# Optimization experiments

Measured on AMD Instinct MI355X. Metric: run time of the kernel, lower is better.

Reference implementation:

```python
import jax, jax.numpy as jnp
import numpy as np

INPUT_DIM = 128
OUTPUT_DIM = 32
H1, H2 = 32, 16

def _lstm(x, Wih, Whh, bih, bhh):
    # x: [B,T,D]; Wih: [4H,D]; Whh: [4H,H]; PyTorch gate order i,f,g,o
    B = x.shape[0]
    H = Whh.shape[1]
    xg = jnp.einsum('btd,gd->btg', x, Wih) + bih + bhh  # precompute input gates [B,T,4H]
    def step(carry, g):
        h, c = carry
        gates = g + h @ Whh.T
        i, f, gg, o = jnp.split(gates, 4, axis=-1)
        c = jax.nn.sigmoid(f) * c + jax.nn.sigmoid(i) * jnp.tanh(gg)
        h = jax.nn.sigmoid(o) * jnp.tanh(c)
        return (h, c), h
    h0 = jnp.zeros((B, H), x.dtype)
    (_, _), hs = jax.lax.scan(step, (h0, h0), jnp.swapaxes(xg, 0, 1))
    return jnp.swapaxes(hs, 0, 1)  # [B,T,H]

def setup_inputs() -> dict:
    key = jax.random.key(0)
    ks = jax.random.split(key, 16)
    def rn(k, shape, scale=0.05):
        return jax.random.normal(k, shape, dtype=jnp.float32) * scale
    d = {}
    d['x'] = jax.random.normal(ks[0], (512, INPUT_DIM, 1024), dtype=jnp.float32)
    d['conv_w'] = rn(ks[1], (INPUT_DIM, INPUT_DIM, 5))
    d['conv_b'] = rn(ks[2], (INPUT_DIM,))
    d['Wih1'] = rn(ks[3], (4 * H1, INPUT_DIM)); d['Whh1'] = rn(ks[4], (4 * H1, H1))
    d['bih1'] = rn(ks[5], (4 * H1,));          d['bhh1'] = rn(ks[6], (4 * H1,))
    d['Wih2'] = rn(ks[7], (4 * H2, H1));       d['Whh2'] = rn(ks[8], (4 * H2, H2))
    d['bih2'] = rn(ks[9], (4 * H2,));          d['bhh2'] = rn(ks[10], (4 * H2,))
    d['Wih3'] = rn(ks[11], (4 * OUTPUT_DIM, H2)); d['Whh3'] = rn(ks[12], (4 * OUTPUT_DIM, OUTPUT_DIM))
    d['bih3'] = rn(ks[13], (4 * OUTPUT_DIM,));    d['bhh3'] = rn(ks[14], (4 * OUTPUT_DIM,))
    return d

def reference(x, conv_w, conv_b, Wih1, Whh1, bih1, bhh1, Wih2, Whh2, bih2, bhh2, Wih3, Whh3, bih3, bhh3):
    B = x.shape[0]
    t = x.reshape(B, INPUT_DIM, -1)
    c = jax.lax.conv_general_dilated(t, conv_w, window_strides=(1,), padding='VALID',
                                     dimension_numbers=('NCH', 'OIH', 'NCH'))
    c = c + conv_b[None, :, None]  # [B, C, L']
    # faithful to torch .view: reshape (not transpose) to [B, L', C]
    seq = c.reshape(B, -1, c.shape[1])
    h1 = _lstm(seq, Wih1, Whh1, bih1, bhh1)
    h2 = _lstm(h1, Wih2, Whh2, bih2, bhh2)
    h3 = _lstm(h2, Wih3, Whh3, bih3, bhh3)
    return h3[:, -1, :]
```

## Files before the change

### kernel.cpp

```cpp
#include <hip/hip_runtime.h>

static constexpr int BATCH = 512;
static constexpr int TT    = 1020;
static constexpr int MM    = BATCH * TT;

typedef __bf16 bf8 __attribute__((ext_vector_type(8)));
typedef float  f4v __attribute__((ext_vector_type(4)));

__device__ __forceinline__ float fsig(float x) {
  float e = __builtin_amdgcn_exp2f(x * -1.442695041f);
  return __builtin_amdgcn_rcpf(1.0f + e);
}
__device__ __forceinline__ float ftanh(float x) {
  float e = __builtin_amdgcn_exp2f(x * 2.885390082f);
  return 1.0f - 2.0f * __builtin_amdgcn_rcpf(e + 1.0f);
}

__device__ __forceinline__ f4v mfma16(bf8 a, bf8 b, f4v c) {
  return __builtin_amdgcn_mfma_f32_16x16x32_bf16(a, b, c, 0, 0, 0);
}

__global__ __launch_bounds__(64) void pack_w_kernel(
    const float* __restrict__ w, ushort* __restrict__ wp) {
  const int lane = threadIdx.x;
  const int ch = blockIdx.x & 3;
  const int ct = (blockIdx.x >> 2) & 7;
  const int k  = blockIdx.x >> 5;
  const int co  = ct * 16 + (lane & 15);
  const int ci0 = ch * 32 + (lane >> 4) * 8;
  ushort hi[8], lo[8];
#pragma unroll
  for (int j = 0; j < 8; ++j) {
    const float v = w[(size_t)(co * 128 + ci0 + j) * 5 + k];
    const unsigned u = __float_as_uint(v);
    const float hf = __uint_as_float(u & 0xffff0000u);
    hi[j] = (ushort)(u >> 16);
    lo[j] = (ushort)(__float_as_uint(v - hf) >> 16);
  }
  ushort* d0 = wp + ((size_t)blockIdx.x * 2 + 0) * 512 + (size_t)lane * 8;
  ushort* d1 = d0 + 512;
#pragma unroll
  for (int j = 0; j < 8; ++j) { d0[j] = hi[j]; d1[j] = lo[j]; }
}

__global__ __launch_bounds__(256) void conv_mfma_kernel(
    const float* __restrict__ x, const ushort* __restrict__ wp,
    const float* __restrict__ bias, float* __restrict__ c) {
  __shared__ ushort xT[2][260][40];
  const int b    = blockIdx.z;
  const int cb   = blockIdx.x;
  const int l0   = blockIdx.y * 256;
  const int tid  = threadIdx.x;
  const int lane = tid & 63;
  const int wv   = tid >> 6;
  const int lrow = lane & 15;
  const int lgrp = lane >> 4;

  f4v acc[4][4];
#pragma unroll
  for (int m = 0; m < 4; ++m)
#pragma unroll
    for (int t = 0; t < 4; ++t) acc[m][t] = (f4v){0.f, 0.f, 0.f, 0.f};

  const int sp  = tid & 15;
  const int slq = tid >> 4;

  for (int ch = 0; ch < 4; ++ch) {
    const int ci0 = ch * 32;
    __syncthreads();
    {
      const float* xr0 = x + ((size_t)b * 128 + ci0 + 2 * sp) * 1024 + l0;
      const float* xr1 = xr0 + 1024;
      for (int j = 0; j < 5; ++j) {
        const int l = slq * 4 + 64 * j;
        if (l >= 260) break;
        const bool ok = (l0 + l) < 1024;
        float4 a0 = make_float4(0.f, 0.f, 0.f, 0.f);
        float4 a1 = make_float4(0.f, 0.f, 0.f, 0.f);
        if (ok) { a0 = *(const float4*)(xr0 + l); a1 = *(const float4*)(xr1 + l); }
        const float v0[4] = {a0.x, a0.y, a0.z, a0.w};
        const float v1[4] = {a1.x, a1.y, a1.z, a1.w};
#pragma unroll
        for (int e = 0; e < 4; ++e) {
          const unsigned u0 = __float_as_uint(v0[e]);
          const unsigned u1 = __float_as_uint(v1[e]);
          const unsigned h0 = u0 & 0xffff0000u;
          const unsigned h1 = u1 & 0xffff0000u;
          const float l0f = v0[e] - __uint_as_float(h0);
          const float l1f = v1[e] - __uint_as_float(h1);
          const unsigned hp = (u0 >> 16) | h1;
          const unsigned lp = (__float_as_uint(l0f) >> 16) |
                              (__float_as_uint(l1f) & 0xffff0000u);
          *(unsigned*)&xT[0][l + e][2 * sp] = hp;
          *(unsigned*)&xT[1][l + e][2 * sp] = lp;
        }
      }
    }
    __syncthreads();
#pragma unroll
    for (int k = 0; k < 5; ++k) {
      bf8 xa[4][2];
#pragma unroll
      for (int m = 0; m < 4; ++m) {
        const int row = wv * 64 + m * 16 + lrow + k;
        xa[m][0] = *(const bf8*)&xT[0][row][lgrp * 8];
        xa[m][1] = *(const bf8*)&xT[1][row][lgrp * 8];
      }
#pragma unroll
      for (int ct = 0; ct < 4; ++ct) {
        const ushort* wf =
            wp + (size_t)(((k * 8 + cb * 4 + ct) * 4 + ch) * 2) * 512 + lane * 8;
        const bf8 wh = *(const bf8*)wf;
        const bf8 wl = *(const bf8*)(wf + 512);
#pragma unroll
        for (int m = 0; m < 4; ++m) {
          acc[m][ct] = mfma16(xa[m][0], wh, acc[m][ct]);
          acc[m][ct] = mfma16(xa[m][1], wh, acc[m][ct]);
          acc[m][ct] = mfma16(xa[m][0], wl, acc[m][ct]);
        }
      }
    }
  }
#pragma unroll
  for (int ct = 0; ct < 4; ++ct) {
    const int co = cb * 64 + ct * 16 + lrow;
    const float bv = bias[co];
    float* crow = c + (size_t)b * 130560 + (size_t)co * TT;
#pragma unroll
    for (int m = 0; m < 4; ++m) {
      const int l = l0 + wv * 64 + m * 16 + lgrp * 4;
      if (l < TT) {
        float4 st;
        st.x = acc[m][ct][0] + bv; st.y = acc[m][ct][1] + bv;
        st.z = acc[m][ct][2] + bv; st.w = acc[m][ct][3] + bv;
        *(float4*)(crow + l) = st;
      }
    }
  }
}

template <int K>
__global__ __launch_bounds__(256) void gemm_xg(
    const float* __restrict__ A, const float* __restrict__ W,
    const float* __restrict__ bih, const float* __restrict__ bhh,
    float* __restrict__ xgT, const int Ntot) {
  constexpr int KC = (K > 64) ? 64 : K;
  constexpr int LITEMS = (16 * KC) / 256 > 0 ? (16 * KC) / 256 : 1;
  __shared__ float At[KC][68];
  __shared__ float Wt[KC][68];
  const int m0 = blockIdx.x * 64;
  const int n0 = blockIdx.y * 64;
  const int tid = threadIdx.x;
  const int tn = tid & 15;
  const int tm = tid >> 4;

  float acc[4][4];
#pragma unroll
  for (int i = 0; i < 4; ++i)
#pragma unroll
    for (int j = 0; j < 4; ++j) acc[i][j] = 0.f;

  for (int kc = 0; kc < K; kc += KC) {
    __syncthreads();
#pragma unroll
    for (int it = 0; it < LITEMS; ++it) {
      const int i  = tid + it * 256;
      const int r  = i / (KC / 4);
      const int c4 = i % (KC / 4);
      const float4 v = *(const float4*)(A + (size_t)(m0 + r) * K + kc + c4 * 4);
      At[c4 * 4 + 0][r] = v.x; At[c4 * 4 + 1][r] = v.y;
      At[c4 * 4 + 2][r] = v.z; At[c4 * 4 + 3][r] = v.w;
    }
#pragma unroll
    for (int it = 0; it < LITEMS; ++it) {
      const int i  = tid + it * 256;
      const int r  = i / (KC / 4);
      const int c4 = i % (KC / 4);
      const float4 v = *(const float4*)(W + (size_t)(n0 + r) * K + kc + c4 * 4);
      Wt[c4 * 4 + 0][r] = v.x; Wt[c4 * 4 + 1][r] = v.y;
      Wt[c4 * 4 + 2][r] = v.z; Wt[c4 * 4 + 3][r] = v.w;
    }
    __syncthreads();
#pragma unroll 8
    for (int k = 0; k < KC; ++k) {
      const float4 av = *(const float4*)&At[k][tm * 4];
      const float4 wv = *(const float4*)&Wt[k][tn * 4];
      const float a[4] = {av.x, av.y, av.z, av.w};
      const float wr[4] = {wv.x, wv.y, wv.z, wv.w};
#pragma unroll
      for (int i = 0; i < 4; ++i)
#pragma unroll
        for (int j = 0; j < 4; ++j)
          acc[i][j] = fmaf(a[i], wr[j], acc[i][j]);
    }
  }
  float bv[4];
#pragma unroll
  for (int j = 0; j < 4; ++j)
    bv[j] = bih[n0 + tn * 4 + j] + bhh[n0 + tn * 4 + j];
#pragma unroll
  for (int i = 0; i < 4; ++i) {
    const int m  = m0 + tm * 4 + i;
    const int bb = (int)(((unsigned long long)m * 4311810306ULL) >> 42);
    const int t  = m - bb * TT;
    float* dst = xgT + ((size_t)bb * Ntot + n0 + tn * 4) * TT + t;
#pragma unroll
    for (int j = 0; j < 4; ++j) dst[(size_t)j * TT] = acc[i][j] + bv[j];
  }
}

template <int H, bool FINAL>
__global__ __launch_bounds__(64) void lstm_kernel(
    const float* __restrict__ xgT, const float* __restrict__ Whh,
    float* __restrict__ hout) {
  constexpr int G   = 4 * H;
  constexpr int GPL = G / 64;
  constexpr int KG  = H / 4;
  const int b    = blockIdx.x;
  const int lane = threadIdx.x;
  const int g0 = lane;
  const int g1 = lane + 64;

  float w0[H];
  float w1[GPL == 2 ? H : 1];
#pragma unroll
  for (int k = 0; k < H; ++k) {
    w0[k] = Whh[g0 * H + k];
    if constexpr (GPL == 2) w1[k] = Whh[g1 * H + k];
  }

  const float* p0 = xgT + ((size_t)b * G + g0) * TT;
  const float* p1 = xgT + ((size_t)b * G + (GPL == 2 ? g1 : g0)) * TT;

  float h = 0.f, c = 0.f;
  float4 cur0[4], cur1[4], nxt0[4], nxt1[4];
#pragma unroll
  for (int r = 0; r < 4; ++r) {
    cur0[r] = *(const float4*)(p0 + 4 * r);
    nxt0[r] = *(const float4*)(p0 + 16 + 4 * r);
    if constexpr (GPL == 2) {
      cur1[r] = *(const float4*)(p1 + 4 * r);
      nxt1[r] = *(const float4*)(p1 + 16 + 4 * r);
    }
  }

  for (int t16 = 0; t16 < TT; t16 += 16) {
#pragma unroll
    for (int r = 0; r < 4; ++r) {
      const int t4 = t16 + 4 * r;
      if (t4 >= TT) break;
#pragma unroll
      for (int s = 0; s < 4; ++s) {
        float q0[4], q1[4];
        q0[0] = ((const float*)&cur0[r])[s]; q0[1] = 0.f; q0[2] = 0.f; q0[3] = 0.f;
        if constexpr (GPL == 2) {
          q1[0] = ((const float*)&cur1[r])[s]; q1[1] = 0.f; q1[2] = 0.f; q1[3] = 0.f;
        }
#pragma unroll
        for (int g = 0; g < 4; ++g)
#pragma unroll
          for (int k8 = 0; k8 < KG; ++k8) {
            const int k = g * KG + k8;
            const float hk =
                __uint_as_float(__builtin_amdgcn_readlane(__float_as_uint(h), k));
            q0[g] = fmaf(w0[k], hk, q0[g]);
            if constexpr (GPL == 2) q1[g] = fmaf(w1[k], hk, q1[g]);
          }
        const float acc0 = (q0[0] + q0[1]) + (q0[2] + q0[3]);
        float acc1 = 0.f;
        if constexpr (GPL == 2) acc1 = (q1[0] + q1[1]) + (q1[2] + q1[3]);

        float iraw, fraw, graw, oraw;
        if constexpr (H == 32) {
          const float r0 = __shfl_xor(acc0, 32, 64);
          const float r1 = __shfl_xor(acc1, 32, 64);
          const bool hi = lane >= 32;
          iraw = hi ? r0 : acc0;
          fraw = hi ? acc0 : r0;
          graw = hi ? r1 : acc1;
          oraw = hi ? acc1 : r1;
        } else {
          const float x1 = __shfl_xor(acc0, 16, 64);
          const float x2 = __shfl_xor(acc0, 32, 64);
          const float x3 = __shfl_xor(acc0, 48, 64);
          const int q = lane >> 4;
          const float t0 = (q & 1) ? x1 : acc0;
          const float t1 = (q & 1) ? acc0 : x1;
          const float u0 = (q & 1) ? x3 : x2;
          const float u1 = (q & 1) ? x2 : x3;
          const bool hi2 = q >= 2;
          iraw = hi2 ? u0 : t0;
          fraw = hi2 ? u1 : t1;
          graw = hi2 ? t0 : u0;
          oraw = hi2 ? t1 : u1;
        }
        const float ig = fsig(iraw);
        const float fg = fsig(fraw);
        const float gg = ftanh(graw);
        const float og = fsig(oraw);
        c = fmaf(fg, c, ig * gg);
        h = og * ftanh(c);
        if constexpr (!FINAL) {
          if (lane < H) hout[((size_t)b * TT + (t4 + s)) * H + lane] = h;
        } else {
          if (t4 + s == TT - 1 && lane < H) hout[b * H + lane] = h;
        }
      }
    }
#pragma unroll
    for (int r = 0; r < 4; ++r) {
      cur0[r] = nxt0[r];
      if constexpr (GPL == 2) cur1[r] = nxt1[r];
      const int tp = t16 + 32 + 4 * r;
      if (tp < TT) {
        nxt0[r] = *(const float4*)(p0 + tp);
        if constexpr (GPL == 2) nxt1[r] = *(const float4*)(p1 + tp);
      }
    }
  }
}

extern "C" void kernel_launch(void* const* d_in, const int* in_sizes, int n_in,
                              void* d_out, int out_size, void* d_ws, size_t ws_size,
                              hipStream_t stream) {
  const float* x      = (const float*)d_in[0];
  const float* conv_w = (const float*)d_in[1];
  const float* conv_b = (const float*)d_in[2];
  const float* Wih1   = (const float*)d_in[3];
  const float* Whh1   = (const float*)d_in[4];
  const float* bih1   = (const float*)d_in[5];
  const float* bhh1   = (const float*)d_in[6];
  const float* Wih2   = (const float*)d_in[7];
  const float* Whh2   = (const float*)d_in[8];
  const float* bih2   = (const float*)d_in[9];
  const float* bhh2   = (const float*)d_in[10];
  const float* Wih3   = (const float*)d_in[11];
  const float* Whh3   = (const float*)d_in[12];
  const float* bih3   = (const float*)d_in[13];
  const float* bhh3   = (const float*)d_in[14];
  float* out = (float*)d_out;
  float* ws  = (float*)d_ws;

  float* c    = ws;
  float* xgT1 = ws + 66846720;
  float* h1   = ws + 133693440;
  float* xgT2 = c;
  float* h2   = h1;
  float* xgT3 = xgT1;
  ushort* wpack = (ushort*)h1;

  pack_w_kernel<<<160, 64, 0, stream>>>(conv_w, wpack);
  conv_mfma_kernel<<<dim3(2, 4, BATCH), 256, 0, stream>>>(x, wpack, conv_b, c);
  gemm_xg<128><<<dim3(MM / 64, 2), 256, 0, stream>>>(c, Wih1, bih1, bhh1, xgT1, 128);
  lstm_kernel<32, false><<<BATCH, 64, 0, stream>>>(xgT1, Whh1, h1);
  gemm_xg<32><<<dim3(MM / 64, 1), 256, 0, stream>>>(h1, Wih2, bih2, bhh2, xgT2, 64);
  lstm_kernel<16, false><<<BATCH, 64, 0, stream>>>(xgT2, Whh2, h2);
  gemm_xg<16><<<dim3(MM / 64, 2), 256, 0, stream>>>(h2, Wih3, bih3, bhh3, xgT3, 128);
  lstm_kernel<32, true><<<BATCH, 64, 0, stream>>>(xgT3, Whh3, out);
}
```

Baseline: 2.271 ms.

## Interleave multiple batch sequences per wavefront in LSTM recurrence kernels

Each LSTM block now processes NC batch elements (4 for H=32, 8 for H=16) with interleaved independent recurrences inside one wavefront, and the grid shrinks by the same factor. The goal is to hide the serial latency of readlane/FMA/transcendental chains by giving the scheduler independent work from other sequences. The input-gate prefetch is restructured into a 3-slot float4 ring buffer, and launch bounds now request one wave per SIMD. The trade-off is far fewer blocks than compute units, plus higher register pressure.

```diff
diff --git a/kernel.cpp b/kernel.cpp
--- a/kernel.cpp
+++ b/kernel.cpp
@@ -209,112 +209,128 @@
   }
 }
 
-template <int H, bool FINAL>
-__global__ __launch_bounds__(64) void lstm_kernel(
+template <int H, int NC, bool FINAL>
+__global__ __launch_bounds__(64, 1) void lstm_kernel(
     const float* __restrict__ xgT, const float* __restrict__ Whh,
     float* __restrict__ hout) {
   constexpr int G   = 4 * H;
   constexpr int GPL = G / 64;
   constexpr int KG  = H / 4;
-  const int b    = blockIdx.x;
+  const int b0   = blockIdx.x * NC;
   const int lane = threadIdx.x;
-  const int g0 = lane;
-  const int g1 = lane + 64;
 
   float w0[H];
   float w1[GPL == 2 ? H : 1];
 #pragma unroll
   for (int k = 0; k < H; ++k) {
-    w0[k] = Whh[g0 * H + k];
-    if constexpr (GPL == 2) w1[k] = Whh[g1 * H + k];
-  }
-
-  const float* p0 = xgT + ((size_t)b * G + g0) * TT;
-  const float* p1 = xgT + ((size_t)b * G + (GPL == 2 ? g1 : g0)) * TT;
-
-  float h = 0.f, c = 0.f;
-  float4 cur0[4], cur1[4], nxt0[4], nxt1[4];
-#pragma unroll
-  for (int r = 0; r < 4; ++r) {
-    cur0[r] = *(const float4*)(p0 + 4 * r);
-    nxt0[r] = *(const float4*)(p0 + 16 + 4 * r);
+    w0[k] = Whh[lane * H + k];
+    if constexpr (GPL == 2) w1[k] = Whh[(lane + 64) * H + k];
+  }
+
+  const float* p0[NC];
+  const float* p1[GPL == 2 ? NC : 1];
+  float hs[NC], cs[NC];
+  float4 buf0[NC][3];
+  float4 buf1[GPL == 2 ? NC : 1][3];
+#pragma unroll
+  for (int cc = 0; cc < NC; ++cc) {
+    p0[cc] = xgT + ((size_t)(b0 + cc) * G + lane) * TT;
+    hs[cc] = 0.f; cs[cc] = 0.f;
+#pragma unroll
+    for (int sl = 0; sl < 3; ++sl)
+      buf0[cc][sl] = *(const float4*)(p0[cc] + 4 * sl);
     if constexpr (GPL == 2) {
-      cur1[r] = *(const float4*)(p1 + 4 * r);
-      nxt1[r] = *(const float4*)(p1 + 16 + 4 * r);
-    }
-  }
-
-  for (int t16 = 0; t16 < TT; t16 += 16) {
-#pragma unroll
-    for (int r = 0; r < 4; ++r) {
-      const int t4 = t16 + 4 * r;
-      if (t4 >= TT) break;
-#pragma unroll
+      p1[cc] = xgT + ((size_t)(b0 + cc) * G + lane + 64) * TT;
+#pragma unroll
+      for (int sl = 0; sl < 3; ++sl)
+        buf1[cc][sl] = *(const float4*)(p1[cc] + 4 * sl);
+    }
+  }
+
+  for (int t12 = 0; t12 < TT; t12 += 12) {
+#pragma unroll
+    for (int sl = 0; sl < 3; ++sl) {
+#pragma unroll 1
       for (int s = 0; s < 4; ++s) {
-        float q0[4], q1[4];
-        q0[0] = ((const float*)&cur0[r])[s]; q0[1] = 0.f; q0[2] = 0.f; q0[3] = 0.f;
-        if constexpr (GPL == 2) {
-          q1[0] = ((const float*)&cur1[r])[s]; q1[1] = 0.f; q1[2] = 0.f; q1[3] = 0.f;
+        const int t = t12 + sl * 4 + s;
+#pragma unroll
+        for (int cc = 0; cc < NC; ++cc) {
+          const float4 v0 = buf0[cc][sl];
+          const float xg0 =
+              (s == 0) ? v0.x : (s == 1) ? v0.y : (s == 2) ? v0.z : v0.w;
+          float xg1 = 0.f;
+          if constexpr (GPL == 2) {
+            const float4 v1 = buf1[cc][sl];
+            xg1 = (s == 0) ? v1.x : (s == 1) ? v1.y : (s == 2) ? v1.z : v1.w;
+          }
+          float q0[4], q1[4];
+          q0[0] = xg0; q0[1] = 0.f; q0[2] = 0.f; q0[3] = 0.f;
+          if constexpr (GPL == 2) {
+            q1[0] = xg1; q1[1] = 0.f; q1[2] = 0.f; q1[3] = 0.f;
+          }
+#pragma unroll
+          for (int g = 0; g < 4; ++g)
+#pragma unroll
+            for (int k8 = 0; k8 < KG; ++k8) {
+              const int k = g * KG + k8;
+              const float hk = __uint_as_float(
+                  __builtin_amdgcn_readlane(__float_as_uint(hs[cc]), k));
+              q0[g] = fmaf(w0[k], hk, q0[g]);
+              if constexpr (GPL == 2) q1[g] = fmaf(w1[k], hk, q1[g]);
+            }
+          const float acc0 = (q0[0] + q0[1]) + (q0[2] + q0[3]);
+          float acc1 = 0.f;
+          if constexpr (GPL == 2) acc1 = (q1[0] + q1[1]) + (q1[2] + q1[3]);
+
+          float iraw, fraw, graw, oraw;
+          if constexpr (H == 32) {
+            const float r0 = __shfl_xor(acc0, 32, 64);
+            const float r1 = __shfl_xor(acc1, 32, 64);
+            const bool hi = lane >= 32;
+            iraw = hi ? r0 : acc0;
+            fraw = hi ? acc0 : r0;
+            graw = hi ? r1 : acc1;
+            oraw = hi ? acc1 : r1;
+          } else {
+            const float x1 = __shfl_xor(acc0, 16, 64);
+            const float x2 = __shfl_xor(acc0, 32, 64);
+            const float x3 = __shfl_xor(acc0, 48, 64);
+            const int q = lane >> 4;
+            const float t0 = (q & 1) ? x1 : acc0;
+            const float t1 = (q & 1) ? acc0 : x1;
+            const float u0 = (q & 1) ? x3 : x2;
+            const float u1 = (q & 1) ? x2 : x3;
+            const bool hi2 = q >= 2;
+            iraw = hi2 ? u0 : t0;
+            fraw = hi2 ? u1 : t1;
+            graw = hi2 ? t0 : u0;
+            oraw = hi2 ? t1 : u1;
+          }
+          const float ig = fsig(iraw);
+          const float fg = fsig(fraw);
+          const float gg = ftanh(graw);
+          const float og = fsig(oraw);
+          cs[cc] = fmaf(fg, cs[cc], ig * gg);
+          hs[cc] = og * ftanh(cs[cc]);
+          if constexpr (!FINAL) {
+            if (lane < H)
+              hout[((size_t)(b0 + cc) * TT + t) * H + lane] = hs[cc];
+          } else {
+            if (t == TT - 1 && lane < H)
+              hout[(b0 + cc) * H + lane] = hs[cc];
+          }
         }
-#pragma unroll
-        for (int g = 0; g < 4; ++g)
-#pragma unroll
-          for (int k8 = 0; k8 < KG; ++k8) {
-            const int k = g * KG + k8;
-            const float hk =
-                __uint_as_float(__builtin_amdgcn_readlane(__float_as_uint(h), k));
-            q0[g] = fmaf(w0[k], hk, q0[g]);
-            if constexpr (GPL == 2) q1[g] = fmaf(w1[k], hk, q1[g]);
-          }
-        const float acc0 = (q0[0] + q0[1]) + (q0[2] + q0[3]);
-        float acc1 = 0.f;
-        if constexpr (GPL == 2) acc1 = (q1[0] + q1[1]) + (q1[2] + q1[3]);
-
-        float iraw, fraw, graw, oraw;
-        if constexpr (H == 32) {
-          const float r0 = __shfl_xor(acc0, 32, 64);
-          const float r1 = __shfl_xor(acc1, 32, 64);
-          const bool hi = lane >= 32;
-          iraw = hi ? r0 : acc0;
-          fraw = hi ? acc0 : r0;
-          graw = hi ? r1 : acc1;
-          oraw = hi ? acc1 : r1;
-        } else {
-          const float x1 = __shfl_xor(acc0, 16, 64);
-          const float x2 = __shfl_xor(acc0, 32, 64);
-          const float x3 = __shfl_xor(acc0, 48, 64);
-          const int q = lane >> 4;
-          const float t0 = (q & 1) ? x1 : acc0;
-          const float t1 = (q & 1) ? acc0 : x1;
-          const float u0 = (q & 1) ? x3 : x2;
-          const float u1 = (q & 1) ? x2 : x3;
-          const bool hi2 = q >= 2;
-          iraw = hi2 ? u0 : t0;
-          fraw = hi2 ? u1 : t1;
-          graw = hi2 ? t0 : u0;
-          oraw = hi2 ? t1 : u1;
+      }
+      {
+        const int tp = t12 + 12 + 4 * sl;
+        if (tp < TT) {
+#pragma unroll
+          for (int cc = 0; cc < NC; ++cc) {
+            buf0[cc][sl] = *(const float4*)(p0[cc] + tp);
+            if constexpr (GPL == 2)
+              buf1[cc][sl] = *(const float4*)(p1[cc] + tp);
+          }
         }
-        const float ig = fsig(iraw);
-        const float fg = fsig(fraw);
-        const float gg = ftanh(graw);
-        const float og = fsig(oraw);
-        c = fmaf(fg, c, ig * gg);
-        h = og * ftanh(c);
-        if constexpr (!FINAL) {
-          if (lane < H) hout[((size_t)b * TT + (t4 + s)) * H + lane] = h;
-        } else {
-          if (t4 + s == TT - 1 && lane < H) hout[b * H + lane] = h;
-        }
-      }
-    }
-#pragma unroll
-    for (int r = 0; r < 4; ++r) {
-      cur0[r] = nxt0[r];
-      if constexpr (GPL == 2) cur1[r] = nxt1[r];
-      const int tp = t16 + 32 + 4 * r;
-      if (tp < TT) {
-        nxt0[r] = *(const float4*)(p0 + tp);
-        if constexpr (GPL == 2) nxt1[r] = *(const float4*)(p1 + tp);
       }
     }
   }
@@ -352,9 +368,9 @@
   pack_w_kernel<<<160, 64, 0, stream>>>(conv_w, wpack);
   conv_mfma_kernel<<<dim3(2, 4, BATCH), 256, 0, stream>>>(x, wpack, conv_b, c);
   gemm_xg<128><<<dim3(MM / 64, 2), 256, 0, stream>>>(c, Wih1, bih1, bhh1, xgT1, 128);
-  lstm_kernel<32, false><<<BATCH, 64, 0, stream>>>(xgT1, Whh1, h1);
+  lstm_kernel<32, 4, false><<<BATCH / 4, 64, 0, stream>>>(xgT1, Whh1, h1);
   gemm_xg<32><<<dim3(MM / 64, 1), 256, 0, stream>>>(h1, Wih2, bih2, bhh2, xgT2, 64);
-  lstm_kernel<16, false><<<BATCH, 64, 0, stream>>>(xgT2, Whh2, h2);
+  lstm_kernel<16, 8, false><<<BATCH / 8, 64, 0, stream>>>(xgT2, Whh2, h2);
   gemm_xg<16><<<dim3(MM / 64, 2), 256, 0, stream>>>(h2, Wih3, bih3, bhh3, xgT3, 128);
-  lstm_kernel<32, true><<<BATCH, 64, 0, stream>>>(xgT3, Whh3, out);
-}
+  lstm_kernel<32, 4, true><<<BATCH / 4, 64, 0, stream>>>(xgT3, Whh3, out);
+}
```

After: 5.469 ms. +140.8%, slower.
